# Optimization experiments

Hardware: AMD Instinct MI355X
Metric: run time of the kernel (lower is better)

## Reference

```python
import jax, jax.numpy as jnp
import numpy as np

B, S, D, H, H2 = 2048, 96, 7, 64, 16  # batch, seq, input/output feat, bilstm hidden, lstm2 hidden


def setup_inputs() -> dict:
    key = jax.random.key(0)
    ks = jax.random.split(key, 32)
    p = lambda i, shape: jax.random.normal(ks[i], shape, jnp.float32) * 0.1
    inp = {
        'x': jax.random.normal(ks[0], (B, S, D), jnp.float32),
        # feature attention linears (D -> D)
        'fv_w': p(1, (D, D)), 'fv_b': p(2, (D,)),
        'fk_w': p(3, (D, D)), 'fk_b': p(4, (D,)),
        'fq_w': p(5, (D, D)), 'fq_b': p(6, (D,)),
        # bidirectional LSTM, forward dir (torch layout: W_ih [4H,D], W_hh [4H,H])
        'l1f_wih': p(7, (4 * H, D)), 'l1f_whh': p(8, (4 * H, H)),
        'l1f_bih': p(9, (4 * H,)), 'l1f_bhh': p(10, (4 * H,)),
        # backward dir
        'l1b_wih': p(11, (4 * H, D)), 'l1b_whh': p(12, (4 * H, H)),
        'l1b_bih': p(13, (4 * H,)), 'l1b_bhh': p(14, (4 * H,)),
        # temporal attention linears (H -> H)
        'tv_w': p(15, (H, H)), 'tv_b': p(16, (H,)),
        'tk_w': p(17, (H, H)), 'tk_b': p(18, (H,)),
        'tq_w': p(19, (H, H)), 'tq_b': p(20, (H,)),
        # lstm2: input H=64 -> hidden H2=16
        'l2_wih': p(21, (4 * H2, H)), 'l2_whh': p(22, (4 * H2, H2)),
        'l2_bih': p(23, (4 * H2,)), 'l2_bhh': p(24, (4 * H2,)),
        # fc: 16 -> 7
        'fc_w': p(25, (D, H2)), 'fc_b': p(26, (D,)),
    }
    return inp


def _run_lstm(x, wih, whh, bih, bhh, reverse=False):
    # x: [B, S, Din]; torch gate order i, f, g, o
    Hh = whh.shape[1]
    xg = jnp.einsum('bsd,gd->sbg', x, wih) + bih + bhh  # [S, B, 4H]
    h0 = jnp.zeros((x.shape[0], Hh), x.dtype)

    def step(carry, gx):
        h, c = carry
        g = gx + h @ whh.T
        i, f, gg, o = jnp.split(g, 4, axis=-1)
        c = jax.nn.sigmoid(f) * c + jax.nn.sigmoid(i) * jnp.tanh(gg)
        h = jax.nn.sigmoid(o) * jnp.tanh(c)
        return (h, c), h

    _, hs = jax.lax.scan(step, (h0, h0), xg, reverse=reverse)
    return jnp.swapaxes(hs, 0, 1)  # [B, S, H]


def _fwd(x, fv_w, fv_b, fk_w, fk_b, fq_w, fq_b,
         l1f_wih, l1f_whh, l1f_bih, l1f_bhh,
         l1b_wih, l1b_whh, l1b_bih, l1b_bhh,
         tv_w, tv_b, tk_w, tk_b, tq_w, tq_b,
         l2_wih, l2_whh, l2_bih, l2_bhh, fc_w, fc_b):
    lin = lambda y, w, b: y @ w.T + b
    # feature attention (over the D=7 feature axis)
    v = lin(x, fv_w, fv_b)
    k = lin(x + v, fk_w, fk_b)
    q = lin(x + k, fq_w, fq_b)
    fatt = jax.nn.softmax(jnp.einsum('bsi,bsj->bij', q, k), axis=-1)  # [B, D, D]
    fa = jnp.tanh(jnp.einsum('bsi,bij->bsj', v, fatt) + x)
    # bidirectional LSTM; concat-view-mean over directions == (hf + hb) / 2
    hf = _run_lstm(fa, l1f_wih, l1f_whh, l1f_bih, l1f_bhh, reverse=False)
    hb = _run_lstm(fa, l1b_wih, l1b_whh, l1b_bih, l1b_bhh, reverse=True)
    lo = 0.5 * (hf + hb)  # [B, S, H]
    # temporal attention (over the S axis)
    tv = lin(lo, tv_w, tv_b)
    tk = lin(lo, tk_w, tk_b)
    tq = lin(lo, tq_w, tq_b)
    tatt = jax.nn.softmax(jnp.einsum('bid,bjd->bij', tq, tk), axis=-1)  # [B, S, S]
    to = jnp.tanh(jnp.einsum('bij,bjd->bid', tatt, tv))
    # second LSTM + fc
    o2 = _run_lstm(to, l2_wih, l2_whh, l2_bih, l2_bhh, reverse=False)  # [B, S, 16]
    return o2 @ fc_w.T + fc_b  # [B, S, D]


def reference(x, fv_w, fv_b, fk_w, fk_b, fq_w, fq_b,
              l1f_wih, l1f_whh, l1f_bih, l1f_bhh,
              l1b_wih, l1b_whh, l1b_bih, l1b_bhh,
              tv_w, tv_b, tk_w, tk_b, tq_w, tq_b,
              l2_wih, l2_whh, l2_bih, l2_bhh, fc_w, fc_b):
    return _fwd(x, fv_w, fv_b, fk_w, fk_b, fq_w, fq_b,
                l1f_wih, l1f_whh, l1f_bih, l1f_bhh,
                l1b_wih, l1b_whh, l1b_bih, l1b_bhh,
                tv_w, tv_b, tk_w, tk_b, tq_w, tq_b,
                l2_wih, l2_whh, l2_bih, l2_bhh, fc_w, fc_b)
```

## Files before the change

kernel.cpp:

```cpp
#include <hip/hip_runtime.h>
#include <math.h>

#define BB 2048
#define SS 96
#define DD 7
#define HH 64
#define H2 16
#define FASTR 776
#define HST2 72
#define LO_ST 72
#define QK_ST 68
#define TV_ST 104
#define P_ST 104
#define HSB 20

typedef _Float16 f16x8 __attribute__((ext_vector_type(8)));
typedef _Float16 f16x4 __attribute__((ext_vector_type(4)));
typedef float f32x4 __attribute__((ext_vector_type(4)));

__device__ __forceinline__ float frcp(float x) { return __builtin_amdgcn_rcpf(x); }
__device__ __forceinline__ float sigm(float x) { return frcp(1.0f + __expf(-x)); }
__device__ __forceinline__ float tanh_f(float x) { return 1.0f - 2.0f * frcp(__expf(2.0f * x) + 1.0f); }
__device__ __forceinline__ float rl(float v, int l) {
    return __int_as_float(__builtin_amdgcn_readlane(__float_as_int(v), l));
}
__device__ __forceinline__ f16x8 frag_from_f32(const float* base) {
    const float4* p = (const float4*)base;
    float4 a = p[0], b = p[1];
    f16x8 r;
    r[0] = (_Float16)a.x; r[1] = (_Float16)a.y; r[2] = (_Float16)a.z; r[3] = (_Float16)a.w;
    r[4] = (_Float16)b.x; r[5] = (_Float16)b.y; r[6] = (_Float16)b.z; r[7] = (_Float16)b.w;
    return r;
}
__device__ __forceinline__ f16x8 ld2x4(const _Float16* p) {
    f16x4 a = *(const f16x4*)p;
    f16x4 b = *(const f16x4*)(p + 4);
    f16x8 r;
    r[0]=a[0]; r[1]=a[1]; r[2]=a[2]; r[3]=a[3];
    r[4]=b[0]; r[5]=b[1]; r[6]=b[2]; r[7]=b[3];
    return r;
}

__global__ __launch_bounds__(256) void k_prep(
    const float* __restrict__ tv_w, const float* __restrict__ tk_w,
    const float* __restrict__ tq_w, const float* __restrict__ l2_wih,
    const float* __restrict__ l2_bih, const float* __restrict__ l2_bhh,
    _Float16* __restrict__ w16, float* __restrict__ bsum)
{
    const int t = blockIdx.x * 256 + threadIdx.x;
    if (t < 4096)       w16[t] = (_Float16)tv_w[t];
    else if (t < 8192)  w16[t] = (_Float16)tk_w[t - 4096];
    else if (t < 12288) w16[t] = (_Float16)tq_w[t - 8192];
    else                w16[t] = (_Float16)l2_wih[t - 12288];
    if (t < 64) bsum[t] = l2_bih[t] + l2_bhh[t];
}

__global__ __launch_bounds__(128) void k_feat(
    const float* __restrict__ x,
    const float* __restrict__ fv_w, const float* __restrict__ fv_b,
    const float* __restrict__ fk_w, const float* __restrict__ fk_b,
    const float* __restrict__ fq_w, const float* __restrict__ fq_b,
    _Float16* __restrict__ fa16)
{
    __shared__ float xs[SS * DD], vs[SS * DD], ks[SS * DD], qs[SS * DD];
    __shared__ float att[DD * DD];
    __shared__ float wv[49], wk[49], wq[49];
    __shared__ float bv[DD], bk[DD], bq[DD];
    const int b = blockIdx.x, t = threadIdx.x;
    const float* xb = x + (size_t)b * SS * DD;

    for (int idx = t; idx < SS * DD; idx += 128) xs[idx] = xb[idx];
    if (t < 49) { wv[t] = fv_w[t]; wk[t] = fk_w[t]; wq[t] = fq_w[t]; }
    if (t < DD) { bv[t] = fv_b[t]; bk[t] = fk_b[t]; bq[t] = fq_b[t]; }
    __syncthreads();

    if (t < SS) {
        float xr[DD], vr[DD], kr[DD];
        #pragma unroll
        for (int i = 0; i < DD; i++) xr[i] = xs[t * DD + i];
        #pragma unroll
        for (int j = 0; j < DD; j++) {
            float a = bv[j];
            #pragma unroll
            for (int i = 0; i < DD; i++) a += xr[i] * wv[j * DD + i];
            vr[j] = a; vs[t * DD + j] = a;
        }
        #pragma unroll
        for (int j = 0; j < DD; j++) {
            float a = bk[j];
            #pragma unroll
            for (int i = 0; i < DD; i++) a += (xr[i] + vr[i]) * wk[j * DD + i];
            kr[j] = a; ks[t * DD + j] = a;
        }
        #pragma unroll
        for (int j = 0; j < DD; j++) {
            float a = bq[j];
            #pragma unroll
            for (int i = 0; i < DD; i++) a += (xr[i] + kr[i]) * wq[j * DD + i];
            qs[t * DD + j] = a;
        }
    }
    __syncthreads();

    if (t < 98) {
        const int g = t >> 1, l = t & 1;
        const int i = g / DD, j = g % DD;
        float a = 0.0f;
        for (int s = l; s < SS; s += 2) a += qs[s * DD + i] * ks[s * DD + j];
        a += __shfl_xor(a, 1);
        if (l == 0) att[g] = a;
    }
    __syncthreads();
    if (t < DD) {
        float m = -1e30f;
        #pragma unroll
        for (int j = 0; j < DD; j++) m = fmaxf(m, att[t * DD + j]);
        float e[DD]; float sum = 0.0f;
        #pragma unroll
        for (int j = 0; j < DD; j++) { e[j] = __expf(att[t * DD + j] - m); sum += e[j]; }
        float inv = frcp(sum);
        #pragma unroll
        for (int j = 0; j < DD; j++) att[t * DD + j] = e[j] * inv;
    }
    __syncthreads();

    if (t < SS) {
        float vr[DD];
        #pragma unroll
        for (int i = 0; i < DD; i++) vr[i] = vs[t * DD + i];
        f16x8 o;
        #pragma unroll
        for (int j = 0; j < DD; j++) {
            float a = xs[t * DD + j];
            #pragma unroll
            for (int i = 0; i < DD; i++) a += vr[i] * att[i * DD + j];
            o[j] = (_Float16)tanh_f(a);
        }
        o[7] = (_Float16)1.0f;
        *(f16x8*)(fa16 + (size_t)b * FASTR + t * 8) = o;
    }
}

__global__ __launch_bounds__(256, 2) void k_bilstm(
    const _Float16* __restrict__ fa16,
    const float* __restrict__ wih_f, const float* __restrict__ whh_f,
    const float* __restrict__ bih_f, const float* __restrict__ bhh_f,
    const float* __restrict__ wih_b, const float* __restrict__ whh_b,
    const float* __restrict__ bih_b, const float* __restrict__ bhh_b,
    _Float16* __restrict__ hf, _Float16* __restrict__ hb)
{
    __shared__ __align__(16) _Float16 faS[16 * FASTR];
    __shared__ __align__(16) _Float16 hS[2][16 * HST2];

    const int bx = blockIdx.x;
    const int bg = bx >> 1, dir = bx & 1;
    const int t = threadIdx.x, lane = t & 63, w = t >> 6;
    const int col = lane & 15, quad = lane >> 4;

    const float* wih = dir ? wih_b : wih_f;
    const float* whh = dir ? whh_b : whh_f;
    const float* bih = dir ? bih_b : bih_f;
    const float* bhh = dir ? bhh_b : bhh_f;
    _Float16* hout = dir ? hb : hf;

    for (int i = t; i < 2 * 16 * HST2 / 2; i += 256) ((unsigned int*)hS)[i] = 0u;

    f16x8 wh[4][2];
    f16x8 wi[4];
    #pragma unroll
    for (int gt = 0; gt < 4; gt++) {
        const int row = 16 * (w + 4 * gt) + col;
        wh[gt][0] = frag_from_f32(whh + row * HH + quad * 8);
        wh[gt][1] = frag_from_f32(whh + row * HH + 32 + quad * 8);
        f16x8 v;
        #pragma unroll
        for (int j = 0; j < 8; j++) v[j] = (_Float16)0.0f;
        if (quad == 0) {
            #pragma unroll
            for (int j = 0; j < DD; j++) v[j] = (_Float16)wih[row * DD + j];
            v[7] = (_Float16)(bih[row] + bhh[row]);
        }
        wi[gt] = v;
    }

    const f16x8* fab = (const f16x8*)(fa16 + (size_t)(bg * 16) * FASTR);
    f16x8* faD = (f16x8*)faS;
    for (int i8 = t; i8 < 16 * FASTR / 8; i8 += 256) faD[i8] = fab[i8];
    __syncthreads();

    const int sstep = dir ? -HH : HH;
    _Float16* hp = hout + ((size_t)(bg * 16 + col)) * SS * HH
                 + (dir ? (SS - 1) : 0) * HH + 16 * w + quad * 4;

    const f32x4 ZC = {0.f, 0.f, 0.f, 0.f};
    float c0 = 0.f, c1 = 0.f, c2 = 0.f, c3 = 0.f;
    f16x4 hq;
    f32x4 gin[4];

    {
        const int s0 = dir ? (SS - 1) : 0;
        f16x8 faf;
        #pragma unroll
        for (int j = 0; j < 8; j++) faf[j] = (_Float16)0.0f;
        if (quad == 0) faf = *(const f16x8*)(&faS[col * FASTR + s0 * 8]);
        #pragma unroll
        for (int gt = 0; gt < 4; gt++)
            gin[gt] = __builtin_amdgcn_mfma_f32_16x16x32_f16(wi[gt], faf, ZC, 0, 0, 0);
    }

    for (int step = 0; step < SS; step++) {
        const int p = step & 1;

        if (step) {
            *(f16x4*)hp = hq;
            hp += sstep;
        }

        f16x8 h0 = *(const f16x8*)(&hS[p][col * HST2 + quad * 8]);
        f16x8 h1 = *(const f16x8*)(&hS[p][col * HST2 + 32 + quad * 8]);

        f32x4 g[4];
        #pragma unroll
        for (int gt = 0; gt < 4; gt++) {
            f32x4 acc = __builtin_amdgcn_mfma_f32_16x16x32_f16(wh[gt][0], h0, gin[gt], 0, 0, 0);
            acc = __builtin_amdgcn_mfma_f32_16x16x32_f16(wh[gt][1], h1, acc, 0, 0, 0);
            g[gt] = acc;
        }
        {
            float iv, fv, gv, ov, hv;
            iv = sigm(g[0][0]); fv = sigm(g[1][0]); gv = tanh_f(g[2][0]); ov = sigm(g[3][0]);
            c0 = fv * c0 + iv * gv; hv = ov * tanh_f(c0); hq[0] = (_Float16)hv;
            iv = sigm(g[0][1]); fv = sigm(g[1][1]); gv = tanh_f(g[2][1]); ov = sigm(g[3][1]);
            c1 = fv * c1 + iv * gv; hv = ov * tanh_f(c1); hq[1] = (_Float16)hv;
            iv = sigm(g[0][2]); fv = sigm(g[1][2]); gv = tanh_f(g[2][2]); ov = sigm(g[3][2]);
            c2 = fv * c2 + iv * gv; hv = ov * tanh_f(c2); hq[2] = (_Float16)hv;
            iv = sigm(g[0][3]); fv = sigm(g[1][3]); gv = tanh_f(g[2][3]); ov = sigm(g[3][3]);
            c3 = fv * c3 + iv * gv; hv = ov * tanh_f(c3); hq[3] = (_Float16)hv;
        }
        *(f16x4*)(&hS[1 - p][col * HST2 + 16 * w + quad * 4]) = hq;

        if (step + 1 < SS) {
            const int sn = dir ? (SS - 2 - step) : (step + 1);
            f16x8 faf;
            #pragma unroll
            for (int j = 0; j < 8; j++) faf[j] = (_Float16)0.0f;
            if (quad == 0) faf = *(const f16x8*)(&faS[col * FASTR + sn * 8]);
            #pragma unroll
            for (int gt = 0; gt < 4; gt++)
                gin[gt] = __builtin_amdgcn_mfma_f32_16x16x32_f16(wi[gt], faf, ZC, 0, 0, 0);
        }
        __syncthreads();
    }
    *(f16x4*)hp = hq;
}

__global__ __launch_bounds__(512, 1) void k_attn(
    const _Float16* __restrict__ hf, const _Float16* __restrict__ hb,
    const float* __restrict__ tv_b, const float* __restrict__ tk_b,
    const float* __restrict__ tq_b,
    const _Float16* __restrict__ w16, const float* __restrict__ bsum,
    _Float16* __restrict__ xg2)
{
    __shared__ __align__(16) _Float16 loB[SS * LO_ST];
    __shared__ __align__(16) _Float16 tvT[HH * TV_ST];
    __shared__ __align__(16) _Float16 uQK[2 * SS * QK_ST];
    _Float16* qS  = uQK;
    _Float16* tkS = uQK + SS * QK_ST;
    _Float16* pS  = uQK;

    const int b = blockIdx.x, t = threadIdx.x;
    const int lane = t & 63, w = t >> 6;
    const int col = lane & 15, quad = lane >> 4;

    f16x8 wf0[9], wf1[9]; float bj9[9];
    #pragma unroll
    for (int i = 0; i < 9; i++) {
        const int flat = w + 8 * i;
        const int proj = flat / 24, rem = flat % 24;
        const int nt = rem & 3;
        const int j = 16 * nt + col;
        const _Float16* wp = w16 + proj * 4096 + j * 64 + quad * 8;
        wf0[i] = *(const f16x8*)wp;
        wf1[i] = *(const f16x8*)(wp + 32);
        const float* bvec = (proj == 0) ? tv_b : (proj == 1) ? tk_b : tq_b;
        bj9[i] = bvec[j];
    }
    f16x8 l2f0[3], l2f1[3]; float bg3[3];
    #pragma unroll
    for (int i = 0; i < 3; i++) {
        const int flat = w + 8 * i;
        const int nt = flat & 3;
        const int g = 16 * nt + col;
        const _Float16* wp = w16 + 12288 + g * 64 + quad * 8;
        l2f0[i] = *(const f16x8*)wp;
        l2f1[i] = *(const f16x8*)(wp + 32);
        bg3[i] = bsum[g];
    }

    const _Float16* hfp = hf + (size_t)b * SS * HH;
    const _Float16* hbp = hb + (size_t)b * SS * HH;
    for (int g8 = t; g8 < 768; g8 += 512) {
        f16x8 va = *(const f16x8*)(hfp + g8 * 8);
        f16x8 vb = *(const f16x8*)(hbp + g8 * 8);
        int s = g8 >> 3, d = (g8 & 7) * 8;
        f16x8 r;
        #pragma unroll
        for (int j = 0; j < 8; j++) r[j] = (_Float16)(0.5f * ((float)va[j] + (float)vb[j]));
        *(f16x8*)(&loB[s * LO_ST + d]) = r;
    }
    __syncthreads();

    #pragma unroll
    for (int i = 0; i < 9; i++) {
        const int flat = w + 8 * i;
        const int proj = flat / 24, rem = flat % 24;
        const int mt = rem >> 2, nt = rem & 3;
        const int j = 16 * nt + col;
        f32x4 acc = {0.f, 0.f, 0.f, 0.f};
        {
            f16x8 a0 = *(const f16x8*)(&loB[(16 * mt + col) * LO_ST + quad * 8]);
            f16x8 a1 = *(const f16x8*)(&loB[(16 * mt + col) * LO_ST + 32 + quad * 8]);
            acc = __builtin_amdgcn_mfma_f32_16x16x32_f16(a0, wf0[i], acc, 0, 0, 0);
            acc = __builtin_amdgcn_mfma_f32_16x16x32_f16(a1, wf1[i], acc, 0, 0, 0);
        }
        const float bj = bj9[i];
        #pragma unroll
        for (int r = 0; r < 4; r++) {
            const float v = acc[r] + bj;
            const int row = 16 * mt + quad * 4 + r;
            if (proj == 0)      tvT[j * TV_ST + row] = (_Float16)v;
            else if (proj == 1) tkS[row * QK_ST + j] = (_Float16)v;
            else                qS[row * QK_ST + j]  = (_Float16)v;
        }
    }
    __syncthreads();

    f32x4 sc[6];
    const int mt = w;
    if (w < 6) {
        f16x8 aq0 = ld2x4(qS + (16 * mt + col) * QK_ST + quad * 8);
        f16x8 aq1 = ld2x4(qS + (16 * mt + col) * QK_ST + 32 + quad * 8);
        #pragma unroll
        for (int nt = 0; nt < 6; nt++) {
            f32x4 acc = {0.f, 0.f, 0.f, 0.f};
            f16x8 b0 = ld2x4(tkS + (16 * nt + col) * QK_ST + quad * 8);
            f16x8 b1 = ld2x4(tkS + (16 * nt + col) * QK_ST + 32 + quad * 8);
            acc = __builtin_amdgcn_mfma_f32_16x16x32_f16(aq0, b0, acc, 0, 0, 0);
            acc = __builtin_amdgcn_mfma_f32_16x16x32_f16(aq1, b1, acc, 0, 0, 0);
            sc[nt] = acc;
        }
    }
    __syncthreads();

    if (w < 6) {
        #pragma unroll
        for (int r = 0; r < 4; r++) {
            float m = sc[0][r];
            #pragma unroll
            for (int nt = 1; nt < 6; nt++) m = fmaxf(m, sc[nt][r]);
            #pragma unroll
            for (int o = 1; o < 16; o <<= 1) m = fmaxf(m, __shfl_xor(m, o));
            float e[6]; float sum = 0.0f;
            #pragma unroll
            for (int nt = 0; nt < 6; nt++) { e[nt] = __expf(sc[nt][r] - m); sum += e[nt]; }
            #pragma unroll
            for (int o = 1; o < 16; o <<= 1) sum += __shfl_xor(sum, o);
            const float inv = frcp(sum);
            const int row = 16 * mt + quad * 4 + r;
            #pragma unroll
            for (int nt = 0; nt < 6; nt++)
                pS[row * P_ST + 16 * nt + col] = (_Float16)(e[nt] * inv);
        }
        f16x8 pa0 = *(const f16x8*)(pS + (16 * mt + col) * P_ST + quad * 8);
        f16x8 pa1 = *(const f16x8*)(pS + (16 * mt + col) * P_ST + 32 + quad * 8);
        f16x8 pa2 = *(const f16x8*)(pS + (16 * mt + col) * P_ST + 64 + quad * 8);
        #pragma unroll
        for (int nt = 0; nt < 4; nt++) {
            f32x4 acc = {0.f, 0.f, 0.f, 0.f};
            const _Float16* tvrow = tvT + (16 * nt + col) * TV_ST;
            acc = __builtin_amdgcn_mfma_f32_16x16x32_f16(pa0, *(const f16x8*)(tvrow + quad * 8), acc, 0, 0, 0);
            acc = __builtin_amdgcn_mfma_f32_16x16x32_f16(pa1, *(const f16x8*)(tvrow + 32 + quad * 8), acc, 0, 0, 0);
            acc = __builtin_amdgcn_mfma_f32_16x16x32_f16(pa2, *(const f16x8*)(tvrow + 64 + quad * 8), acc, 0, 0, 0);
            #pragma unroll
            for (int r = 0; r < 4; r++)
                loB[(16 * mt + quad * 4 + r) * LO_ST + 16 * nt + col] = (_Float16)tanh_f(acc[r]);
        }
    }
    __syncthreads();

    #pragma unroll
    for (int i = 0; i < 3; i++) {
        const int flat = w + 8 * i;
        const int mt2 = flat >> 2, nt = flat & 3;
        const int g = 16 * nt + col;
        f32x4 acc = {0.f, 0.f, 0.f, 0.f};
        {
            f16x8 a0 = *(const f16x8*)(&loB[(16 * mt2 + col) * LO_ST + quad * 8]);
            f16x8 a1 = *(const f16x8*)(&loB[(16 * mt2 + col) * LO_ST + 32 + quad * 8]);
            acc = __builtin_amdgcn_mfma_f32_16x16x32_f16(a0, l2f0[i], acc, 0, 0, 0);
            acc = __builtin_amdgcn_mfma_f32_16x16x32_f16(a1, l2f1[i], acc, 0, 0, 0);
        }
        const float bg2 = bg3[i];
        #pragma unroll
        for (int r = 0; r < 4; r++) {
            const int row = 16 * mt2 + quad * 4 + r;
            xg2[(size_t)b * SS * HH + row * HH + g] = (_Float16)(acc[r] + bg2);
        }
    }
}

__global__ __launch_bounds__(256) void k_lstm2(
    const _Float16* __restrict__ xg2,
    const float* __restrict__ l2_whh,
    const float* __restrict__ fc_w, const float* __restrict__ fc_b,
    float* __restrict__ out)
{
    __shared__ _Float16 hsb[4][SS * HSB];

    const int t = threadIdx.x, lane = t & 63, w = t >> 6;
    const int n = blockIdx.x * 4 + w;
    const int u16 = lane & 15;

    float whr[H2];
    #pragma unroll
    for (int j = 0; j < H2; j++) whr[j] = l2_whh[lane * H2 + j];

    const _Float16* xgp = xg2 + (size_t)n * SS * HH + lane;
    float h = 0.0f, c = 0.0f;
    _Float16 xv = xgp[0];

    for (int s = 0; s < SS; s++) {
        _Float16 xnext = (_Float16)0.0f;
        if (s + 1 < SS) xnext = xgp[(s + 1) * HH];

        float a0 = (float)xv, a1 = 0.0f, a2 = 0.0f, a3 = 0.0f;
        #pragma unroll
        for (int j = 0; j < H2; j += 4) {
            a0 += rl(h, j)     * whr[j];
            a1 += rl(h, j + 1) * whr[j + 1];
            a2 += rl(h, j + 2) * whr[j + 2];
            a3 += rl(h, j + 3) * whr[j + 3];
        }
        float a = (a0 + a1) + (a2 + a3);
        float iv = __shfl(a, u16);
        float fv = __shfl(a, H2 + u16);
        float gv = __shfl(a, 2 * H2 + u16);
        float ov = __shfl(a, 3 * H2 + u16);
        c = sigm(fv) * c + sigm(iv) * tanh_f(gv);
        h = sigm(ov) * tanh_f(c);
        if (lane < H2) hsb[w][s * HSB + lane] = (_Float16)h;
        xv = xnext;
    }
    __syncthreads();

    for (int s = lane; s < SS; s += 64) {
        float hr[H2];
        #pragma unroll
        for (int j = 0; j < H2; j++) hr[j] = (float)hsb[w][s * HSB + j];
        float* op = out + ((size_t)n * SS + s) * DD;
        #pragma unroll
        for (int d = 0; d < DD; d++) {
            float a = fc_b[d];
            #pragma unroll
            for (int j = 0; j < H2; j++) a += hr[j] * fc_w[d * H2 + j];
            op[d] = a;
        }
    }
}

extern "C" void kernel_launch(void* const* d_in, const int* in_sizes, int n_in,
                              void* d_out, int out_size, void* d_ws, size_t ws_size,
                              hipStream_t stream) {
    const float* x     = (const float*)d_in[0];
    const float* fv_w  = (const float*)d_in[1];
    const float* fv_b  = (const float*)d_in[2];
    const float* fk_w  = (const float*)d_in[3];
    const float* fk_b  = (const float*)d_in[4];
    const float* fq_w  = (const float*)d_in[5];
    const float* fq_b  = (const float*)d_in[6];
    const float* l1f_wih = (const float*)d_in[7];
    const float* l1f_whh = (const float*)d_in[8];
    const float* l1f_bih = (const float*)d_in[9];
    const float* l1f_bhh = (const float*)d_in[10];
    const float* l1b_wih = (const float*)d_in[11];
    const float* l1b_whh = (const float*)d_in[12];
    const float* l1b_bih = (const float*)d_in[13];
    const float* l1b_bhh = (const float*)d_in[14];
    const float* tv_w  = (const float*)d_in[15];
    const float* tv_b  = (const float*)d_in[16];
    const float* tk_w  = (const float*)d_in[17];
    const float* tk_b  = (const float*)d_in[18];
    const float* tq_w  = (const float*)d_in[19];
    const float* tq_b  = (const float*)d_in[20];
    const float* l2_wih = (const float*)d_in[21];
    const float* l2_whh = (const float*)d_in[22];
    const float* l2_bih = (const float*)d_in[23];
    const float* l2_bhh = (const float*)d_in[24];
    const float* fc_w  = (const float*)d_in[25];
    const float* fc_b  = (const float*)d_in[26];

    _Float16* fa16 = (_Float16*)d_ws;
    _Float16* hf = fa16 + (size_t)BB * FASTR;
    _Float16* hb = hf + (size_t)BB * SS * HH;
    _Float16* w16 = hb + (size_t)BB * SS * HH;
    float* bsum = (float*)(w16 + 16384);
    _Float16* xg2 = hf;

    k_prep<<<64, 256, 0, stream>>>(tv_w, tk_w, tq_w, l2_wih, l2_bih, l2_bhh, w16, bsum);
    k_feat<<<BB, 128, 0, stream>>>(x, fv_w, fv_b, fk_w, fk_b, fq_w, fq_b, fa16);
    k_bilstm<<<256, 256, 0, stream>>>(fa16,
        l1f_wih, l1f_whh, l1f_bih, l1f_bhh,
        l1b_wih, l1b_whh, l1b_bih, l1b_bhh, hf, hb);
    k_attn<<<BB, 512, 0, stream>>>(hf, hb,
        tv_b, tk_b, tq_b, w16, bsum, xg2);
    k_lstm2<<<512, 256, 0, stream>>>(xg2, l2_whh, fc_w, fc_b, (float*)d_out);
}
```

Baseline: 249.3 us.

## Fuse second LSTM and fc into attention kernel to drop xg2 round trip

Removes the separate k_lstm2 kernel. The attention kernel now writes the lstm2 input gates into shared memory instead of global memory. A single wave per block then runs the 96-step recurrence, and all threads compute the fc output. This avoids writing and reading the xg2 intermediate through global memory and saves one launch. In exchange, each attention block has a long serial tail where only one of its eight waves does work, which can lower throughput unless other blocks on the same CU hide it.

Result: slower. 427.7 us (+71.6%).

```diff
diff --git a/kernel.cpp b/kernel.cpp
--- a/kernel.cpp
+++ b/kernel.cpp
@@ -12,7 +12,6 @@
 #define QK_ST 68
 #define TV_ST 104
 #define P_ST 104
-#define HSB 20
 
 typedef _Float16 f16x8 __attribute__((ext_vector_type(8)));
 typedef _Float16 f16x4 __attribute__((ext_vector_type(4)));
@@ -259,14 +258,19 @@
     const float* __restrict__ tv_b, const float* __restrict__ tk_b,
     const float* __restrict__ tq_b,
     const _Float16* __restrict__ w16, const float* __restrict__ bsum,
-    _Float16* __restrict__ xg2)
+    const float* __restrict__ l2_whh,
+    const float* __restrict__ fc_w, const float* __restrict__ fc_b,
+    float* __restrict__ out)
 {
     __shared__ __align__(16) _Float16 loB[SS * LO_ST];
     __shared__ __align__(16) _Float16 tvT[HH * TV_ST];
     __shared__ __align__(16) _Float16 uQK[2 * SS * QK_ST];
+    __shared__ float fcwS[DD * H2];
+    __shared__ float fcbS[DD];
     _Float16* qS  = uQK;
     _Float16* tkS = uQK + SS * QK_ST;
     _Float16* pS  = uQK;
+    _Float16* gS  = uQK;
 
     const int b = blockIdx.x, t = threadIdx.x;
     const int lane = t & 63, w = t >> 6;
@@ -296,6 +300,13 @@
         l2f1[i] = *(const f16x8*)(wp + 32);
         bg3[i] = bsum[g];
     }
+    float whr[H2];
+    if (t < 64) {
+        #pragma unroll
+        for (int j = 0; j < H2; j++) whr[j] = l2_whh[lane * H2 + j];
+    }
+    if (t < DD * H2) fcwS[t] = fc_w[t];
+    if (t < DD)      fcbS[t] = fc_b[t];
 
     const _Float16* hfp = hf + (size_t)b * SS * HH;
     const _Float16* hbp = hb + (size_t)b * SS * HH;
@@ -404,67 +415,42 @@
         #pragma unroll
         for (int r = 0; r < 4; r++) {
             const int row = 16 * mt2 + quad * 4 + r;
-            xg2[(size_t)b * SS * HH + row * HH + g] = (_Float16)(acc[r] + bg2);
-        }
-    }
-}
-
-__global__ __launch_bounds__(256) void k_lstm2(
-    const _Float16* __restrict__ xg2,
-    const float* __restrict__ l2_whh,
-    const float* __restrict__ fc_w, const float* __restrict__ fc_b,
-    float* __restrict__ out)
-{
-    __shared__ _Float16 hsb[4][SS * HSB];
-
-    const int t = threadIdx.x, lane = t & 63, w = t >> 6;
-    const int n = blockIdx.x * 4 + w;
-    const int u16 = lane & 15;
-
-    float whr[H2];
-    #pragma unroll
-    for (int j = 0; j < H2; j++) whr[j] = l2_whh[lane * H2 + j];
-
-    const _Float16* xgp = xg2 + (size_t)n * SS * HH + lane;
-    float h = 0.0f, c = 0.0f;
-    _Float16 xv = xgp[0];
-
-    for (int s = 0; s < SS; s++) {
-        _Float16 xnext = (_Float16)0.0f;
-        if (s + 1 < SS) xnext = xgp[(s + 1) * HH];
-
-        float a0 = (float)xv, a1 = 0.0f, a2 = 0.0f, a3 = 0.0f;
-        #pragma unroll
-        for (int j = 0; j < H2; j += 4) {
-            a0 += rl(h, j)     * whr[j];
-            a1 += rl(h, j + 1) * whr[j + 1];
-            a2 += rl(h, j + 2) * whr[j + 2];
-            a3 += rl(h, j + 3) * whr[j + 3];
-        }
-        float a = (a0 + a1) + (a2 + a3);
-        float iv = __shfl(a, u16);
-        float fv = __shfl(a, H2 + u16);
-        float gv = __shfl(a, 2 * H2 + u16);
-        float ov = __shfl(a, 3 * H2 + u16);
-        c = sigm(fv) * c + sigm(iv) * tanh_f(gv);
-        h = sigm(ov) * tanh_f(c);
-        if (lane < H2) hsb[w][s * HSB + lane] = (_Float16)h;
-        xv = xnext;
-    }
-    __syncthreads();
-
-    for (int s = lane; s < SS; s += 64) {
-        float hr[H2];
-        #pragma unroll
-        for (int j = 0; j < H2; j++) hr[j] = (float)hsb[w][s * HSB + j];
-        float* op = out + ((size_t)n * SS + s) * DD;
-        #pragma unroll
-        for (int d = 0; d < DD; d++) {
-            float a = fc_b[d];
-            #pragma unroll
-            for (int j = 0; j < H2; j++) a += hr[j] * fc_w[d * H2 + j];
-            op[d] = a;
-        }
+            gS[row * HH + g] = (_Float16)(acc[r] + bg2);
+        }
+    }
+    __syncthreads();
+
+    _Float16* hh = loB;
+    if (t < 64) {
+        const int u16 = lane & 15;
+        float h = 0.0f, c = 0.0f;
+        for (int s = 0; s < SS; s++) {
+            float a0 = (float)gS[s * HH + lane], a1 = 0.0f, a2 = 0.0f, a3 = 0.0f;
+            #pragma unroll
+            for (int j = 0; j < H2; j += 4) {
+                a0 += rl(h, j)     * whr[j];
+                a1 += rl(h, j + 1) * whr[j + 1];
+                a2 += rl(h, j + 2) * whr[j + 2];
+                a3 += rl(h, j + 3) * whr[j + 3];
+            }
+            float a = (a0 + a1) + (a2 + a3);
+            float iv = __shfl(a, u16);
+            float fv = __shfl(a, H2 + u16);
+            float gv = __shfl(a, 2 * H2 + u16);
+            float ov = __shfl(a, 3 * H2 + u16);
+            c = sigm(fv) * c + sigm(iv) * tanh_f(gv);
+            h = sigm(ov) * tanh_f(c);
+            if (lane < H2) hh[s * H2 + lane] = (_Float16)h;
+        }
+    }
+    __syncthreads();
+
+    for (int idx = t; idx < SS * DD; idx += 512) {
+        const int s = idx / DD, d = idx % DD;
+        float a = fcbS[d];
+        #pragma unroll
+        for (int j = 0; j < H2; j++) a += (float)hh[s * H2 + j] * fcwS[d * H2 + j];
+        out[((size_t)b * SS + s) * DD + d] = a;
     }
 }
 
@@ -504,7 +490,6 @@
     _Float16* hb = hf + (size_t)BB * SS * HH;
     _Float16* w16 = hb + (size_t)BB * SS * HH;
     float* bsum = (float*)(w16 + 16384);
-    _Float16* xg2 = hf;
 
     k_prep<<<64, 256, 0, stream>>>(tv_w, tk_w, tq_w, l2_wih, l2_bih, l2_bhh, w16, bsum);
     k_feat<<<BB, 128, 0, stream>>>(x, fv_w, fv_b, fk_w, fk_b, fq_w, fq_b, fa16);
@@ -512,6 +497,6 @@
         l1f_wih, l1f_whh, l1f_bih, l1f_bhh,
         l1b_wih, l1b_whh, l1b_bih, l1b_bhh, hf, hb);
     k_attn<<<BB, 512, 0, stream>>>(hf, hb,
-        tv_b, tk_b, tq_b, w16, bsum, xg2);
-    k_lstm2<<<512, 256, 0, stream>>>(xg2, l2_whh, fc_w, fc_b, (float*)d_out);
-}
+        tv_b, tk_b, tq_b, w16, bsum,
+        l2_whh, fc_w, fc_b, (float*)d_out);
+}
```
